# Optimization experiments

Hardware: AMD Instinct MI355X
Metric: run time of the kernel (lower is better)

Reference implementation:

```python
import jax, jax.numpy as jnp
import numpy as np

EMB = 300
NUM_LAYERS = 5
NUM_GRAPHS = 1024
NUM_JUNCTIONS = 8192
TEMP = 0.04
EPS = 1e-5
SELF_LOOP_BOND_TYPE = 4


def gcn_conv(x, edge_index, edge_attr, W, b, ee1, ee2):
    # pretrain-gnns GCNConv: add self-loops (bond type 4, direction 0),
    # degree-normalized add aggregation of (x_src + edge_emb).
    N = x.shape[0]
    loop = jnp.arange(N, dtype=edge_index.dtype)
    src = jnp.concatenate([edge_index[0], loop])
    dst = jnp.concatenate([edge_index[1], loop])
    bt = jnp.concatenate([edge_attr[:, 0], jnp.full((N,), SELF_LOOP_BOND_TYPE, edge_attr.dtype)])
    bd = jnp.concatenate([edge_attr[:, 1], jnp.zeros((N,), edge_attr.dtype)])
    eemb = ee1[bt] + ee2[bd]                                   # [E+N, D]
    deg = jax.ops.segment_sum(jnp.ones(src.shape, x.dtype), src, num_segments=N)
    dinv = jnp.where(deg > 0, 1.0 / jnp.sqrt(jnp.maximum(deg, 1e-12)), 0.0)
    norm = dinv[src] * dinv[dst]                               # [E+N]
    h = x @ W.T + b                                            # [N, D]
    msg = norm[:, None] * (h[src] + eemb)                      # gather + fuse
    return jax.ops.segment_sum(msg, dst, num_segments=N)      # scatter-add


def batchnorm(h, gamma, beta):
    mu = h.mean(0)
    var = h.var(0)
    return gamma * (h - mu) / jnp.sqrt(var + EPS) + beta


def gnn_encoder(x, edge_index, edge_attr, ae1, ae2, W, b, ee1, ee2, gamma, beta):
    h = ae1[x[:, 0]] + ae2[x[:, 1]]
    for l in range(NUM_LAYERS):
        h = gcn_conv(h, edge_index, edge_attr, W[l], b[l], ee1[l], ee2[l])
        h = batchnorm(h, gamma[l], beta[l])
        if l < NUM_LAYERS - 1:
            h = jax.nn.relu(h)
    return h


def junction_encoder(h, jW, jb, jee1, jee2):
    # SuperEncoder is called with empty edge_index -> only self-loops.
    empty_ei = jnp.zeros((2, 0), jnp.int32)
    empty_ea = jnp.zeros((0, 2), jnp.int32)
    h = jax.nn.relu(gcn_conv(h, empty_ei, empty_ea, jW[0], jb[0], jee1[0], jee2[0]))
    return gcn_conv(h, empty_ei, empty_ea, jW[1], jb[1], jee1[1], jee2[1])


def mean_pool(h, ids, num):
    s = jax.ops.segment_sum(h, ids, num_segments=num)
    c = jax.ops.segment_sum(jnp.ones((h.shape[0],), h.dtype), ids, num_segments=num)
    return s / jnp.maximum(c, 1.0)[:, None]


def l2norm(h):
    return h / jnp.maximum(jnp.linalg.norm(h, axis=1, keepdims=True), 1e-12)


def setup_inputs() -> dict:
    key = jax.random.key(0)
    ks = jax.random.split(key, 32)
    N, E = 200000, 400000
    inp = {
        'batch_x': jax.random.randint(ks[0], (N, 2), 0, 3, jnp.int32),
        'batch_edge_index': jax.random.randint(ks[1], (2, E), 0, N, jnp.int32),
        'batch_edge_attr': jax.random.randint(ks[2], (E, 2), 0, 3, jnp.int32),
        'batch_graph_ids': jax.random.randint(ks[3], (N,), 0, NUM_GRAPHS, jnp.int32),
        'frag_x': jax.random.randint(ks[4], (N, 2), 0, 3, jnp.int32),
        'frag_edge_index': jax.random.randint(ks[5], (2, E), 0, N, jnp.int32),
        'frag_edge_attr': jax.random.randint(ks[6], (E, 2), 0, 3, jnp.int32),
        'frag_junction_ids': jax.random.randint(ks[7], (N,), 0, NUM_JUNCTIONS, jnp.int32),
        'junction_graph_ids': jax.random.randint(ks[8], (NUM_JUNCTIONS,), 0, NUM_GRAPHS, jnp.int32),
        'junction_mask': jax.random.uniform(ks[9], (NUM_JUNCTIONS,), jnp.float32),
    }
    s = 0.05
    inp.update({
        'atom_emb1': jax.random.normal(ks[10], (120, EMB), jnp.float32) * s,
        'atom_emb2': jax.random.normal(ks[11], (3, EMB), jnp.float32) * s,
        'gnn_W': jax.random.normal(ks[12], (NUM_LAYERS, EMB, EMB), jnp.float32) * s,
        'gnn_b': jnp.zeros((NUM_LAYERS, EMB), jnp.float32),
        'gnn_ee1': jax.random.normal(ks[13], (NUM_LAYERS, 6, EMB), jnp.float32) * s,
        'gnn_ee2': jax.random.normal(ks[14], (NUM_LAYERS, 3, EMB), jnp.float32) * s,
        'bn_gamma': jnp.ones((NUM_LAYERS, EMB), jnp.float32),
        'bn_beta': jnp.zeros((NUM_LAYERS, EMB), jnp.float32),
        'jct_W': jax.random.normal(ks[15], (2, EMB, EMB), jnp.float32) * s,
        'jct_b': jnp.zeros((2, EMB), jnp.float32),
        'jct_ee1': jax.random.normal(ks[16], (2, 6, EMB), jnp.float32) * s,
        'jct_ee2': jax.random.normal(ks[17], (2, 3, EMB), jnp.float32) * s,
        'mask_embedding': jax.random.normal(ks[18], (EMB,), jnp.float32),
    })
    return inp


def reference(batch_x, batch_edge_index, batch_edge_attr, batch_graph_ids,
              frag_x, frag_edge_index, frag_edge_attr, frag_junction_ids,
              junction_graph_ids, junction_mask,
              atom_emb1, atom_emb2, gnn_W, gnn_b, gnn_ee1, gnn_ee2,
              bn_gamma, bn_beta, jct_W, jct_b, jct_ee1, jct_ee2, mask_embedding):
    # branch 0: whole molecules
    h = gnn_encoder(batch_x, batch_edge_index, batch_edge_attr,
                    atom_emb1, atom_emb2, gnn_W, gnn_b, gnn_ee1, gnn_ee2, bn_gamma, bn_beta)
    g = mean_pool(h, batch_graph_ids, NUM_GRAPHS)
    f0 = l2norm(junction_encoder(g, jct_W, jct_b, jct_ee1, jct_ee2))
    # branch 1: fragments -> junction nodes, masked overwrite, pooled per graph
    h = gnn_encoder(frag_x, frag_edge_index, frag_edge_attr,
                    atom_emb1, atom_emb2, gnn_W, gnn_b, gnn_ee1, gnn_ee2, bn_gamma, bn_beta)
    j = mean_pool(h, frag_junction_ids, NUM_JUNCTIONS)
    j = jnp.where(junction_mask[:, None] > 0.5, mask_embedding[None, :], j)
    j = junction_encoder(j, jct_W, jct_b, jct_ee1, jct_ee2)
    f1 = l2norm(mean_pool(j, junction_graph_ids, NUM_GRAPHS))
    logits = (f0 @ f1.T) / TEMP
    return logits
```

## Files before the change

kernel.cpp:

```cpp
#include <hip/hip_runtime.h>
#include <math.h>

#define EMBD 300
#define HROW 304
#define LDF  304
#define KEXT 320
#define BCH  80
#define BSTR 40
#define TS2  312
#define SPR  608
#define CE(a,b) (((a)+(b)-1)/(b))

typedef _Float16 h16;
typedef __attribute__((ext_vector_type(8))) _Float16 half8;
typedef __attribute__((ext_vector_type(4))) float f32x4;

__global__ void k_diag(float* out, int n, float v){
  int i = blockIdx.x*256 + threadIdx.x;
  if (i < n) out[i] = v;
}
__global__ void k_set_val(int* p, int n, int v){
  int i = blockIdx.x*256 + threadIdx.x;
  if (i < n) p[i] = v;
}
__global__ void k_count_src(const int* __restrict__ ei, int E, int* __restrict__ deg){
  int e = blockIdx.x*256 + threadIdx.x;
  if (e < E) atomicAdd(&deg[ei[e]], 1);
}
__global__ void k_dinv(const int* __restrict__ deg, float* __restrict__ dinv, int N){
  int i = blockIdx.x*256 + threadIdx.x;
  if (i < N) dinv[i] = 1.0f / sqrtf((float)(deg[i] + 1));
}
__global__ void k_count_dst(const int* __restrict__ ei, int E, int* __restrict__ counts){
  int e = blockIdx.x*256 + threadIdx.x;
  if (e < E) atomicAdd(&counts[ei[E + e]], 1);
}
__global__ void k_count_ids(const int* __restrict__ ids, int n, int* __restrict__ counts){
  int i = blockIdx.x*256 + threadIdx.x;
  if (i < n) atomicAdd(&counts[ids[i]], 1);
}
__global__ void k_scan_block(const int* __restrict__ in, int M, int* __restrict__ out, int* __restrict__ bsum){
  __shared__ int s[256];
  int t = threadIdx.x, i = blockIdx.x*256 + t;
  int v = (i < M) ? in[i] : 0;
  s[t] = v; __syncthreads();
  for (int off = 1; off < 256; off <<= 1){
    int x = (t >= off) ? s[t-off] : 0;
    __syncthreads();
    s[t] += x;
    __syncthreads();
  }
  if (i < M) out[i] = s[t] - v;
  if (t == 255) bsum[blockIdx.x] = s[255];
}
__global__ void k_scan_sums(int* __restrict__ bsum, int B){
  __shared__ int s[1024];
  int t = threadIdx.x;
  int v = (t < B) ? bsum[t] : 0;
  s[t] = v; __syncthreads();
  for (int off = 1; off < 1024; off <<= 1){
    int x = (t >= off) ? s[t-off] : 0;
    __syncthreads();
    s[t] += x;
    __syncthreads();
  }
  if (t < B) bsum[t] = s[t] - v;
}
__global__ void k_scan_add(int* __restrict__ out, const int* __restrict__ bsum, int M){
  int i = blockIdx.x*256 + threadIdx.x;
  if (i < M) out[i] += bsum[blockIdx.x];
}
__global__ void k_fill_edges(const int* __restrict__ ei, const int* __restrict__ ea, int E, int N,
                             const int* __restrict__ offs, int* __restrict__ cur, int* __restrict__ entries){
  int e = blockIdx.x*256 + threadIdx.x;
  if (e < E){
    int s  = ei[e];
    int d  = ei[E + e];
    int bt = ea[2*e], bd = ea[2*e + 1];
    int pos = offs[d] + atomicAdd(&cur[d], 1);
    entries[pos] = s | (bt << 20) | (bd << 23);
  } else if (e < E + N){
    int i = e - E;
    int pos = offs[i] + atomicAdd(&cur[i], 1);
    entries[pos] = i | (4 << 20);
  }
}
__global__ void k_fill_rows(const int* __restrict__ ids, int n, const int* __restrict__ offs,
                            int* __restrict__ cur, int* __restrict__ entries){
  int i = blockIdx.x*256 + threadIdx.x;
  if (i < n){
    int g = ids[i];
    int pos = offs[g] + atomicAdd(&cur[g], 1);
    entries[pos] = i;
  }
}

__global__ void k_init_h0(const int* __restrict__ x, const float* __restrict__ ae1,
                          const float* __restrict__ ae2, h16* __restrict__ h, int N){
  int i = blockIdx.x, t = threadIdx.x;
  int a = x[2*i], b = x[2*i + 1];
  const float* e1 = ae1 + (size_t)a*EMBD;
  const float* e2 = ae2 + (size_t)b*EMBD;
  h16* hr = h + (size_t)i*HROW;
  hr[t] = (h16)(e1[t] + e2[t]);
  int c = t + 256;
  if (c < HROW) hr[c] = (c < EMBD) ? (h16)(e1[c] + e2[c]) : (h16)0.f;
}

__global__ void k_wext(const float* __restrict__ W, const float* __restrict__ b,
                       const float* __restrict__ ee1, const float* __restrict__ ee2,
                       h16* __restrict__ out){
  int l = blockIdx.y, o = blockIdx.x, t = threadIdx.x;
  h16* d = out + ((size_t)l*KEXT + o)*KEXT;
  for (int k = t; k < KEXT; k += 256){
    float v = 0.f;
    if (o < EMBD){
      if      (k < EMBD)            v = W[(size_t)l*EMBD*EMBD + (size_t)o*EMBD + k];
      else if (k == 304)            v = b[l*EMBD + o];
      else if (k >= 305 && k < 311) v = ee1[((size_t)l*6 + (k-305))*EMBD + o];
      else if (k >= 311 && k < 314) v = ee2[((size_t)l*3 + (k-311))*EMBD + o];
    }
    d[k] = (h16)v;
  }
}

__global__ void k_id_coef(float* coef, h16* coefh){
  int c = blockIdx.x*256 + threadIdx.x;
  if (c < HROW){
    coef[c] = (c < EMBD) ? 1.f : 0.f;
    coef[HROW + c] = 0.f;
  }
  if (c < KEXT){
    coefh[c] = (c < EMBD) ? (h16)1.f : (h16)0.f;
    coefh[KEXT + c] = (h16)0.f;
  }
}
__global__ void k_bn_coef(const float* __restrict__ stats, const float* __restrict__ gamma,
                          const float* __restrict__ beta, float* __restrict__ coef,
                          h16* __restrict__ coefh, float invN){
  int c = blockIdx.x*256 + threadIdx.x;
  if (c >= KEXT) return;
  float sc = 0.f, sh = 0.f;
  if (c < EMBD){
    float mu  = stats[c]*invN;
    float var = stats[EMBD + c]*invN - mu*mu;
    sc = gamma[c]*rsqrtf(var + 1e-5f);
    sh = beta[c] - mu*sc;
  }
  if (c < HROW){ coef[c] = sc; coef[HROW + c] = sh; }
  coefh[c] = (h16)sc; coefh[KEXT + c] = (h16)sh;
}

__global__ void k_red_stats(const h16* __restrict__ spart, int nb, float* __restrict__ stats){
  int t = threadIdx.x;
  int c1 = t + 256;
  float a0 = 0.f, q0 = 0.f, a1 = 0.f, q1 = 0.f;
  for (int b = blockIdx.x; b < nb; b += gridDim.x){
    const h16* sp = spart + (size_t)b*SPR;
    a0 += (float)sp[t];
    q0 += (float)sp[304 + t];
    if (c1 < EMBD){ a1 += (float)sp[c1]; q1 += (float)sp[304 + c1]; }
  }
  if (t < EMBD){ atomicAdd(&stats[t], a0); atomicAdd(&stats[EMBD + t], q0); }
  if (c1 < EMBD){ atomicAdd(&stats[c1], a1); atomicAdd(&stats[EMBD + c1], q1); }
}

template<int RELU>
__global__ void __launch_bounds__(256)
k_layer(const h16* __restrict__ hRaw, const h16* __restrict__ coefh,
        const float* __restrict__ dinv,
        const int* __restrict__ offs, const int* __restrict__ counts,
        const int* __restrict__ entries, const h16* __restrict__ Wx,
        h16* __restrict__ hOut, int N, h16* __restrict__ spart)
{
  __shared__ h16  tile[64][TS2];
  __shared__ h16  Bs[BCH][BSTR];
  __shared__ float sred[2*HROW];
  __shared__ int   rstart[64];
  __shared__ int   rcnt[64];
  __shared__ float dvv[64];

  int tid = threadIdx.x;
  int wid = tid >> 6, lane = tid & 63;
  int m16 = lane & 15, ko = lane >> 4;
  long row0 = (long)blockIdx.x * 64;

  if (tid < 64){
    long g = row0 + tid;
    int o = 0, c = 0; float d = 0.f;
    if (g < N){ o = offs[g]; c = counts[g]; d = dinv[g]; }
    rstart[tid] = o; rcnt[tid] = c; dvv[tid] = d;
  }
  for (int i = tid; i < 2*HROW; i += 256) sred[i] = 0.f;
  __syncthreads();

  int lr = wid*16 + m16;
  int myStart = rstart[lr], myCnt = rcnt[lr];
  float di = dvv[lr];

  int srcA[8]; float wvA[8]; int eA[8];
  #pragma unroll
  for (int j = 0; j < 8; j++){
    int e = entries[myStart + j];
    bool act = j < myCnt;
    int s = act ? (e & 0xFFFFF) : N;
    float wv = dinv[act ? s : 0];
    wvA[j] = act ? wv : 0.f;
    srcA[j] = s; eA[j] = e;
  }
  float ext[8] = {0,0,0,0,0,0,0,0};
  if (ko >= 2){
    int extbase = (ko - 2)*8;
    #pragma unroll
    for (int j = 0; j < 8; j++){
      unsigned msk = 1u | (1u << (1 + ((eA[j] >> 20) & 7))) | (1u << (7 + ((eA[j] >> 23) & 3)));
      #pragma unroll
      for (int c = 0; c < 8; c++)
        ext[c] += ((msk >> (extbase + c)) & 1u) ? wvA[j] : 0.f;
    }
  }
  half8 wvh[8];
  #pragma unroll
  for (int j = 0; j < 8; j++){
    _Float16 w = (_Float16)wvA[j];
    #pragma unroll
    for (int c = 0; c < 8; c++) wvh[j][c] = w;
  }

  half8 acc[10];
  #pragma unroll
  for (int k = 0; k < 10; k++) acc[k] = (half8)(_Float16)0;

  if (__any(myCnt > 8)){
    for (int j = 8; j < myCnt; j++){
      int e = entries[myStart + j];
      int s = e & 0xFFFFF;
      float wv = dinv[s];
      if (ko >= 2){
        int extbase = (ko - 2)*8;
        unsigned msk = 1u | (1u << (1 + ((e >> 20) & 7))) | (1u << (7 + ((e >> 23) & 3)));
        #pragma unroll
        for (int c = 0; c < 8; c++)
          ext[c] += ((msk >> (extbase + c)) & 1u) ? wv : 0.f;
      }
      _Float16 wh = (_Float16)wv;
      half8 w8;
      #pragma unroll
      for (int c = 0; c < 8; c++) w8[c] = wh;
      #pragma unroll
      for (int k = 0; k < 10; k++){
        if (k == 9 && ko >= 2) break;
        half8 sck = *(const half8*)&coefh[k*32 + ko*8];
        half8 shk = *(const half8*)&coefh[KEXT + k*32 + ko*8];
        half8 x = *(const half8*)(hRaw + (size_t)s*HROW + k*32 + ko*8);
        half8 y = sck*x + shk;
        if (RELU){
          #pragma unroll
          for (int c = 0; c < 8; c++) y[c] = y[c] > (_Float16)0 ? y[c] : (_Float16)0;
        }
        acc[k] += w8*y;
      }
    }
  }

  #pragma unroll
  for (int k = 0; k < 9; k++){
    half8 sck = *(const half8*)&coefh[k*32 + ko*8];
    half8 shk = *(const half8*)&coefh[KEXT + k*32 + ko*8];
    half8 a = acc[k];
    #pragma unroll
    for (int j = 0; j < 8; j++){
      half8 x = *(const half8*)(hRaw + (size_t)srcA[j]*HROW + k*32 + ko*8);
      half8 y = sck*x + shk;
      if (RELU){
        #pragma unroll
        for (int c = 0; c < 8; c++) y[c] = y[c] > (_Float16)0 ? y[c] : (_Float16)0;
      }
      a += wvh[j]*y;
    }
    acc[k] = a;
  }
  {
    half8 a = acc[9];
    if (ko < 2){
      half8 sck = *(const half8*)&coefh[288 + ko*8];
      half8 shk = *(const half8*)&coefh[KEXT + 288 + ko*8];
      #pragma unroll
      for (int j = 0; j < 8; j++){
        half8 x = *(const half8*)(hRaw + (size_t)srcA[j]*HROW + 288 + ko*8);
        half8 y = sck*x + shk;
        if (RELU){
          #pragma unroll
          for (int c = 0; c < 8; c++) y[c] = y[c] > (_Float16)0 ? y[c] : (_Float16)0;
        }
        a += wvh[j]*y;
      }
    } else {
      #pragma unroll
      for (int c = 0; c < 8; c++) a[c] += (_Float16)ext[c];
    }
    acc[9] = a;
  }

  half8 afr[10];
  {
    _Float16 dh = (_Float16)di;
    half8 d8;
    #pragma unroll
    for (int c = 0; c < 8; c++) d8[c] = dh;
    #pragma unroll
    for (int k = 0; k < 10; k++) afr[k] = acc[k] * d8;
  }

  int cr = ko * 4;
  #pragma unroll
  for (int jt = 0; jt < 4; jt++){
    f32x4 a2[5];
    #pragma unroll
    for (int j = 0; j < 5; j++) a2[j] = (f32x4){0.f,0.f,0.f,0.f};
    for (int k0 = 0; k0 < 10; k0++){
      __syncthreads();
      for (int idx = tid; idx < 320; idx += 256){
        int o = idx >> 2, qd = (idx & 3) * 8;
        *(half8*)&Bs[o][qd] = *(const half8*)(Wx + (size_t)(jt*BCH + o)*KEXT + k0*32 + qd);
      }
      __syncthreads();
      #pragma unroll
      for (int j = 0; j < 5; j++){
        half8 bfr = *(const half8*)&Bs[j*16 + m16][ko*8];
        a2[j] = __builtin_amdgcn_mfma_f32_16x16x32_f16(afr[k0], bfr, a2[j], 0, 0, 0);
      }
    }
    #pragma unroll
    for (int j = 0; j < 5; j++){
      int col = jt*BCH + j*16 + m16;
      float s = 0.f, q = 0.f;
      #pragma unroll
      for (int r = 0; r < 4; r++){
        float v = a2[j][r];
        s += v; q += v*v;
      }
      s += __shfl_xor(s, 16, 64); s += __shfl_xor(s, 32, 64);
      q += __shfl_xor(q, 16, 64); q += __shfl_xor(q, 32, 64);
      if (ko == 0 && col < EMBD){
        atomicAdd(&sred[col], s);
        atomicAdd(&sred[HROW + col], q);
      }
    }
    #pragma unroll
    for (int j = 0; j < 5; j++){
      int col = jt*BCH + j*16 + m16;
      if (col < HROW){
        #pragma unroll
        for (int r = 0; r < 4; r++)
          tile[wid*16 + cr + r][col] = (h16)a2[j][r];
      }
    }
  }
  __syncthreads();
  for (int idx = tid; idx < 64*38; idx += 256){
    int row = idx / 38, c = idx - row*38;
    long grow = row0 + row;
    if (grow < N)
      *(uint4*)(hOut + grow*HROW + c*8) = *(const uint4*)&tile[row][c*8];
  }
  h16* sp = spart + (size_t)blockIdx.x*SPR;
  for (int c = tid; c < EMBD; c += 256){
    sp[c]       = (h16)sred[c];
    sp[304 + c] = (h16)sred[HROW + c];
  }
}

__global__ void k_pool_h(const h16* __restrict__ h, const int* __restrict__ offs,
                         const int* __restrict__ counts, const int* __restrict__ entries,
                         float* __restrict__ out, int M){
  int g = blockIdx.x, t = threadIdx.x, c1 = t + 256;
  int off = offs[g], cnt = counts[g];
  float a0 = 0.f, a1 = 0.f;
  for (int j = 0; j < cnt; j++){
    int r = entries[off + j];
    const h16* hr = h + (size_t)r*HROW;
    a0 += (float)hr[t];
    if (c1 < EMBD) a1 += (float)hr[c1];
  }
  float inv = 1.0f / fmaxf((float)cnt, 1.0f);
  float* o = out + (size_t)g*LDF;
  o[t] = a0*inv;
  if (c1 < EMBD) o[c1] = a1*inv;
}
__global__ void k_pool_f32(const float* __restrict__ h, const int* __restrict__ offs,
                           const int* __restrict__ counts, const int* __restrict__ entries,
                           float* __restrict__ out, int M){
  int g = blockIdx.x, t = threadIdx.x, c1 = t + 256;
  int off = offs[g], cnt = counts[g];
  float a0 = 0.f, a1 = 0.f;
  for (int j = 0; j < cnt; j++){
    int r = entries[off + j];
    const float* hr = h + (size_t)r*LDF;
    a0 += hr[t];
    if (c1 < EMBD) a1 += hr[c1];
  }
  float inv = 1.0f / fmaxf((float)cnt, 1.0f);
  float* o = out + (size_t)g*LDF;
  o[t] = a0*inv;
  if (c1 < EMBD) o[c1] = a1*inv;
}

__global__ void k_affine_rows(float* __restrict__ rows, const float* __restrict__ coef, int M){
  int g = blockIdx.x, t = threadIdx.x, c1 = t + 256;
  float* r = rows + (size_t)g*LDF;
  r[t] = coef[t]*r[t] + coef[HROW + t];
  if (c1 < EMBD) r[c1] = coef[c1]*r[c1] + coef[HROW + c1];
}

__global__ void k_mask(float* __restrict__ j, const float* __restrict__ mask,
                       const float* __restrict__ memb, int M){
  int i = blockIdx.x;
  if (mask[i] <= 0.5f) return;
  int t = threadIdx.x, c1 = t + 256;
  float* jr = j + (size_t)i*LDF;
  jr[t] = memb[t];
  if (c1 < EMBD) jr[c1] = memb[c1];
}

__global__ void k_l2norm(float* __restrict__ f, int M){
  int g = blockIdx.x, t = threadIdx.x, c1 = t + 256;
  float* fr = f + (size_t)g*LDF;
  float v0 = fr[t];
  float v1 = (c1 < EMBD) ? fr[c1] : 0.f;
  float ss = v0*v0 + v1*v1;
  #pragma unroll
  for (int o = 32; o > 0; o >>= 1) ss += __shfl_down(ss, o, 64);
  __shared__ float red[4];
  int wid = t >> 6, lane = t & 63;
  if (lane == 0) red[wid] = ss;
  __syncthreads();
  if (t == 0) red[0] = 1.0f / fmaxf(sqrtf(red[0]+red[1]+red[2]+red[3]), 1e-12f);
  __syncthreads();
  float inv = red[0];
  fr[t] = v0*inv;
  if (c1 < EMBD) fr[c1] = v1*inv;
}

__global__ void __launch_bounds__(256)
k_gemm(const float* __restrict__ A, int lda, const float* __restrict__ W, int ldw,
       const float* __restrict__ bias, const float* __restrict__ e1, const float* __restrict__ e2,
       float* __restrict__ C, int ldc, int M, int Ncols, int K, int relu, float scale){
  __shared__ float As[16][68];
  __shared__ float Ws[16][68];
  int row0 = blockIdx.y * 64, col0 = blockIdx.x * 64;
  int tid = threadIdx.x;
  int tx = tid & 15, ty = tid >> 4;
  float acc[4][4] = {};
  for (int k0 = 0; k0 < K; k0 += 16){
    int r  = tid >> 2;
    int kk = (tid & 3) * 4;
    int gk = k0 + kk;
    float v[4] = {0.f,0.f,0.f,0.f};
    int gr = row0 + r;
    if (gr < M){
      if (gk + 3 < K){ float4 f = *(const float4*)(A + (size_t)gr*lda + gk); v[0]=f.x;v[1]=f.y;v[2]=f.z;v[3]=f.w; }
      else for (int j = 0; j < 4; j++) if (gk + j < K) v[j] = A[(size_t)gr*lda + gk + j];
    }
    As[kk+0][r]=v[0]; As[kk+1][r]=v[1]; As[kk+2][r]=v[2]; As[kk+3][r]=v[3];
    float w[4] = {0.f,0.f,0.f,0.f};
    int o = col0 + r;
    if (o < Ncols){
      if (gk + 3 < K){ float4 f = *(const float4*)(W + (size_t)o*ldw + gk); w[0]=f.x;w[1]=f.y;w[2]=f.z;w[3]=f.w; }
      else for (int j = 0; j < 4; j++) if (gk + j < K) w[j] = W[(size_t)o*ldw + gk + j];
    }
    Ws[kk+0][r]=w[0]; Ws[kk+1][r]=w[1]; Ws[kk+2][r]=w[2]; Ws[kk+3][r]=w[3];
    __syncthreads();
    #pragma unroll
    for (int k = 0; k < 16; k++){
      float4 a4 = *(const float4*)&As[k][ty*4];
      float4 b4 = *(const float4*)&Ws[k][tx*4];
      float a[4] = {a4.x,a4.y,a4.z,a4.w};
      float b[4] = {b4.x,b4.y,b4.z,b4.w};
      #pragma unroll
      for (int i = 0; i < 4; i++)
        #pragma unroll
        for (int j = 0; j < 4; j++) acc[i][j] += a[i]*b[j];
    }
    __syncthreads();
  }
  #pragma unroll
  for (int i = 0; i < 4; i++){
    int rr = row0 + ty*4 + i;
    if (rr >= M) continue;
    #pragma unroll
    for (int j = 0; j < 4; j++){
      int cc = col0 + tx*4 + j;
      if (cc >= Ncols) continue;
      float v = acc[i][j];
      if (bias) v += bias[cc];
      if (e1)   v += e1[cc];
      if (e2)   v += e2[cc];
      v *= scale;
      if (relu) v = fmaxf(v, 0.f);
      C[(size_t)rr*ldc + cc] = v;
    }
  }
}

static inline void scan_excl(const int* counts, int M, int* offs, int* bsum, hipStream_t s){
  int B = CE(M, 256);
  k_scan_block<<<B,256,0,s>>>(counts, M, offs, bsum);
  k_scan_sums<<<1,1024,0,s>>>(bsum, B);
  k_scan_add<<<B,256,0,s>>>(offs, bsum, M);
}
static inline void gemm_f32(const float* A,int lda,const float* W,int ldw,
                            const float* bias,const float* e1,const float* e2,
                            float* C,int ldc,int M,int Ncols,int K,
                            int relu,float scale,hipStream_t s){
  dim3 grid(CE(Ncols,64), CE(M,64));
  k_gemm<<<grid,256,0,s>>>(A,lda,W,ldw,bias,e1,e2,C,ldc,M,Ncols,K,relu,scale);
}

extern "C" void kernel_launch(void* const* d_in, const int* in_sizes, int n_in,
                              void* d_out, int out_size, void* d_ws, size_t ws_size,
                              hipStream_t stream) {
  const int*   batch_x   = (const int*)d_in[0];
  const int*   batch_ei  = (const int*)d_in[1];
  const int*   batch_ea  = (const int*)d_in[2];
  const int*   batch_gid = (const int*)d_in[3];
  const int*   frag_x    = (const int*)d_in[4];
  const int*   frag_ei   = (const int*)d_in[5];
  const int*   frag_ea   = (const int*)d_in[6];
  const int*   frag_jid  = (const int*)d_in[7];
  const int*   jct_gid   = (const int*)d_in[8];
  const float* jct_mask  = (const float*)d_in[9];
  const float* ae1       = (const float*)d_in[10];
  const float* ae2       = (const float*)d_in[11];
  const float* gnn_W     = (const float*)d_in[12];
  const float* gnn_b     = (const float*)d_in[13];
  const float* gnn_ee1   = (const float*)d_in[14];
  const float* gnn_ee2   = (const float*)d_in[15];
  const float* bn_gamma  = (const float*)d_in[16];
  const float* bn_beta   = (const float*)d_in[17];
  const float* jct_W     = (const float*)d_in[18];
  const float* jct_b     = (const float*)d_in[19];
  const float* jct_ee1   = (const float*)d_in[20];
  const float* jct_ee2   = (const float*)d_in[21];
  const float* mask_emb  = (const float*)d_in[22];

  const int N = in_sizes[0] / 2;
  const int E = in_sizes[1] / 2;
  const int NG = 1024, NJ = 8192;
  const int LBLK = CE(N, 64);

  size_t off = 0;
  char* base = (char*)d_ws;
  auto carve = [&](size_t bytes) -> void* {
    void* p = base + off;
    off += (bytes + 255) & ~(size_t)255;
    return p;
  };
  h16*  hA      = (h16*) carve((size_t)(N+1) * HROW * 2);
  h16*  hB      = (h16*) carve((size_t)(N+1) * HROW * 2);
  float* dinv    = (float*)carve((size_t)N * 4);
  int*   degcnt  = (int*)  carve((size_t)N * 4);
  int*   cursor  = degcnt;
  int*   counts  = (int*)  carve((size_t)N * 4);
  int*   offs    = (int*)  carve((size_t)(N + 1) * 4);
  int*   entries = (int*)  carve((size_t)(E + N) * 4);
  int*   bsum    = (int*)  carve(1024 * 4);
  float* stats   = (float*)carve(2 * EMBD * 4);
  float* coef    = (float*)carve(2 * HROW * 4);
  float* idcoef  = (float*)carve(2 * HROW * 4);
  h16*  coefh   = (h16*) carve(2 * KEXT * 2);
  h16*  idcoefh = (h16*) carve(2 * KEXT * 2);
  h16*  wext    = (h16*) carve((size_t)5 * KEXT * KEXT * 2);
  float* f0      = (float*)carve((size_t)NG * LDF * 4);
  float* f1      = (float*)carve((size_t)NG * LDF * 4);
  h16*  spart   = (h16*) carve((size_t)LBLK * SPR * 2);
  size_t required = off;
  float* g0      = (float*)hA;
  float* t1      = (float*)((char*)hA + ((size_t)16 << 20));
  float* t2      = (float*)((char*)hA + ((size_t)32 << 20));
  (void)n_in;

  if (ws_size < required || d_ws == nullptr){
    float v = 1.0e6f + (float)(ws_size >> 20) * 1000.0f;
    k_diag<<<CE(out_size,256),256,0,stream>>>((float*)d_out, out_size, v);
    return;
  }

  { dim3 g(KEXT, 5); k_wext<<<g,256,0,stream>>>(gnn_W, gnn_b, gnn_ee1, gnn_ee2, wext); }
  k_id_coef<<<CE(KEXT,256),256,0,stream>>>(idcoef, idcoefh);
  hipMemsetAsync(hA + (size_t)N*HROW, 0, HROW*2, stream);
  hipMemsetAsync(hB + (size_t)N*HROW, 0, HROW*2, stream);

  for (int br = 0; br < 2; br++){
    const int* x  = br ? frag_x  : batch_x;
    const int* ei = br ? frag_ei : batch_ei;
    const int* ea = br ? frag_ea : batch_ea;

    hipMemsetAsync(degcnt, 0, (size_t)N*4, stream);
    k_count_src<<<CE(E,256),256,0,stream>>>(ei, E, degcnt);
    k_dinv<<<CE(N,256),256,0,stream>>>(degcnt, dinv, N);

    k_set_val<<<CE(N,256),256,0,stream>>>(counts, N, 1);
    k_count_dst<<<CE(E,256),256,0,stream>>>(ei, E, counts);
    scan_excl(counts, N, offs, bsum, stream);
    hipMemsetAsync(cursor, 0, (size_t)N*4, stream);
    k_fill_edges<<<CE(E+N,256),256,0,stream>>>(ei, ea, E, N, offs, cursor, entries);

    k_init_h0<<<N,256,0,stream>>>(x, ae1, ae2, hA, N);

    for (int l = 0; l < 5; l++){
      const h16* src = (l & 1) ? hB : hA;
      h16*       dst = (l & 1) ? hA : hB;
      const h16* ch  = (l == 0) ? idcoefh : coefh;
      hipMemsetAsync(stats, 0, 2*EMBD*4, stream);
      if (l == 0)
        k_layer<0><<<LBLK,256,0,stream>>>(src, ch, dinv, offs, counts, entries,
                                          wext + (size_t)l*KEXT*KEXT, dst, N, spart);
      else
        k_layer<1><<<LBLK,256,0,stream>>>(src, ch, dinv, offs, counts, entries,
                                          wext + (size_t)l*KEXT*KEXT, dst, N, spart);
      k_red_stats<<<64,256,0,stream>>>(spart, LBLK, stats);
      k_bn_coef<<<CE(KEXT,256),256,0,stream>>>(stats, bn_gamma + l*EMBD, bn_beta + l*EMBD,
                                               coef, coefh, 1.0f/(float)N);
    }

    if (br == 0){
      hipMemsetAsync(counts, 0, (size_t)NG*4, stream);
      k_count_ids<<<CE(N,256),256,0,stream>>>(batch_gid, N, counts);
      scan_excl(counts, NG, offs, bsum, stream);
      hipMemsetAsync(cursor, 0, (size_t)NG*4, stream);
      k_fill_rows<<<CE(N,256),256,0,stream>>>(batch_gid, N, offs, cursor, entries);
      k_pool_h<<<NG,256,0,stream>>>(hB, offs, counts, entries, g0, NG);
      k_affine_rows<<<NG,256,0,stream>>>(g0, coef, NG);
      gemm_f32(g0, LDF, jct_W, EMBD, jct_b,
               jct_ee1 + 4*EMBD, jct_ee2,
               t1, LDF, NG, EMBD, EMBD, 1, 1.0f, stream);
      gemm_f32(t1, LDF, jct_W + EMBD*EMBD, EMBD, jct_b + EMBD,
               jct_ee1 + 6*EMBD + 4*EMBD, jct_ee2 + 3*EMBD,
               f0, LDF, NG, EMBD, EMBD, 0, 1.0f, stream);
      k_l2norm<<<NG,256,0,stream>>>(f0, NG);
    } else {
      hipMemsetAsync(counts, 0, (size_t)NJ*4, stream);
      k_count_ids<<<CE(N,256),256,0,stream>>>(frag_jid, N, counts);
      scan_excl(counts, NJ, offs, bsum, stream);
      hipMemsetAsync(cursor, 0, (size_t)NJ*4, stream);
      k_fill_rows<<<CE(N,256),256,0,stream>>>(frag_jid, N, offs, cursor, entries);
      k_pool_h<<<NJ,256,0,stream>>>(hB, offs, counts, entries, t1, NJ);
      k_affine_rows<<<NJ,256,0,stream>>>(t1, coef, NJ);
      k_mask<<<NJ,256,0,stream>>>(t1, jct_mask, mask_emb, NJ);
      gemm_f32(t1, LDF, jct_W, EMBD, jct_b,
               jct_ee1 + 4*EMBD, jct_ee2,
               t2, LDF, NJ, EMBD, EMBD, 1, 1.0f, stream);
      gemm_f32(t2, LDF, jct_W + EMBD*EMBD, EMBD, jct_b + EMBD,
               jct_ee1 + 6*EMBD + 4*EMBD, jct_ee2 + 3*EMBD,
               t1, LDF, NJ, EMBD, EMBD, 0, 1.0f, stream);
      hipMemsetAsync(counts, 0, (size_t)NG*4, stream);
      k_count_ids<<<CE(NJ,256),256,0,stream>>>(jct_gid, NJ, counts);
      scan_excl(counts, NG, offs, bsum, stream);
      hipMemsetAsync(cursor, 0, (size_t)NG*4, stream);
      k_fill_rows<<<CE(NJ,256),256,0,stream>>>(jct_gid, NJ, offs, cursor, entries);
      k_pool_f32<<<NG,256,0,stream>>>(t1, offs, counts, entries, f1, NG);
      k_l2norm<<<NG,256,0,stream>>>(f1, NG);
    }
  }

  gemm_f32(f0, LDF, f1, LDF, nullptr, nullptr, nullptr,
           (float*)d_out, 1024, NG, NG, EMBD, 0, 25.0f, stream);
}
```

Baseline: 4.033 ms.

## Use MFMA fp16 GEMM for junction layers and fuse pool/affine/mask kernels

Replaces the fp32 scalar GEMMs in the junction encoder with an MFMA f16 kernel that keeps A fragments in registers and uses padded fp16 copies of the junction weights. It also fuses the BN affine transform and the mask overwrite into the pooling kernel, unrolls the pooling gather by four, and merges the source- and destination-degree counting into one kernel. This cuts launch count and the extra memory passes over the pooled rows, at the cost of fp16 rounding on the junction GEMM inputs.

```diff
diff --git a/kernel.cpp b/kernel.cpp
--- a/kernel.cpp
+++ b/kernel.cpp
@@ -23,17 +23,17 @@
   int i = blockIdx.x*256 + threadIdx.x;
   if (i < n) p[i] = v;
 }
-__global__ void k_count_src(const int* __restrict__ ei, int E, int* __restrict__ deg){
+__global__ void k_count_both(const int* __restrict__ ei, int E,
+                             int* __restrict__ deg, int* __restrict__ cnts){
   int e = blockIdx.x*256 + threadIdx.x;
-  if (e < E) atomicAdd(&deg[ei[e]], 1);
+  if (e < E){
+    atomicAdd(&deg[ei[e]], 1);
+    atomicAdd(&cnts[ei[E + e]], 1);
+  }
 }
 __global__ void k_dinv(const int* __restrict__ deg, float* __restrict__ dinv, int N){
   int i = blockIdx.x*256 + threadIdx.x;
   if (i < N) dinv[i] = 1.0f / sqrtf((float)(deg[i] + 1));
-}
-__global__ void k_count_dst(const int* __restrict__ ei, int E, int* __restrict__ counts){
-  int e = blockIdx.x*256 + threadIdx.x;
-  if (e < E) atomicAdd(&counts[ei[E + e]], 1);
 }
 __global__ void k_count_ids(const int* __restrict__ ids, int n, int* __restrict__ counts){
   int i = blockIdx.x*256 + threadIdx.x;
@@ -122,6 +122,12 @@
     }
     d[k] = (h16)v;
   }
+}
+__global__ void k_wpad(const float* __restrict__ W, h16* __restrict__ out){
+  int l = blockIdx.y, o = blockIdx.x, t = threadIdx.x;
+  h16* d = out + ((size_t)l*KEXT + o)*KEXT;
+  for (int k = t; k < KEXT; k += 256)
+    d[k] = (h16)((o < EMBD && k < EMBD) ? W[(size_t)l*EMBD*EMBD + (size_t)o*EMBD + k] : 0.f);
 }
 
 __global__ void k_id_coef(float* coef, h16* coefh){
@@ -373,20 +379,44 @@
 
 __global__ void k_pool_h(const h16* __restrict__ h, const int* __restrict__ offs,
                          const int* __restrict__ counts, const int* __restrict__ entries,
-                         float* __restrict__ out, int M){
+                         float* __restrict__ out, const float* __restrict__ coef,
+                         const float* __restrict__ mask, const float* __restrict__ memb){
   int g = blockIdx.x, t = threadIdx.x, c1 = t + 256;
   int off = offs[g], cnt = counts[g];
   float a0 = 0.f, a1 = 0.f;
-  for (int j = 0; j < cnt; j++){
+  int j = 0;
+  for (; j + 4 <= cnt; j += 4){
+    int r0 = entries[off+j],   r1 = entries[off+j+1];
+    int r2 = entries[off+j+2], r3 = entries[off+j+3];
+    const h16* p0 = h + (size_t)r0*HROW;
+    const h16* p1 = h + (size_t)r1*HROW;
+    const h16* p2 = h + (size_t)r2*HROW;
+    const h16* p3 = h + (size_t)r3*HROW;
+    float x0 = (float)p0[t], x1 = (float)p1[t];
+    float x2 = (float)p2[t], x3 = (float)p3[t];
+    a0 += (x0 + x1) + (x2 + x3);
+    if (c1 < EMBD){
+      float y0 = (float)p0[c1], y1 = (float)p1[c1];
+      float y2 = (float)p2[c1], y3 = (float)p3[c1];
+      a1 += (y0 + y1) + (y2 + y3);
+    }
+  }
+  for (; j < cnt; j++){
     int r = entries[off + j];
     const h16* hr = h + (size_t)r*HROW;
     a0 += (float)hr[t];
     if (c1 < EMBD) a1 += (float)hr[c1];
   }
   float inv = 1.0f / fmaxf((float)cnt, 1.0f);
+  float v0 = coef[t]*(a0*inv) + coef[HROW + t];
+  float v1 = (c1 < EMBD) ? coef[c1]*(a1*inv) + coef[HROW + c1] : 0.f;
+  if (mask && mask[g] > 0.5f){
+    v0 = memb[t];
+    if (c1 < EMBD) v1 = memb[c1];
+  }
   float* o = out + (size_t)g*LDF;
-  o[t] = a0*inv;
-  if (c1 < EMBD) o[c1] = a1*inv;
+  o[t] = v0;
+  if (c1 < EMBD) o[c1] = v1;
 }
 __global__ void k_pool_f32(const float* __restrict__ h, const int* __restrict__ offs,
                            const int* __restrict__ counts, const int* __restrict__ entries,
@@ -406,23 +436,6 @@
   if (c1 < EMBD) o[c1] = a1*inv;
 }
 
-__global__ void k_affine_rows(float* __restrict__ rows, const float* __restrict__ coef, int M){
-  int g = blockIdx.x, t = threadIdx.x, c1 = t + 256;
-  float* r = rows + (size_t)g*LDF;
-  r[t] = coef[t]*r[t] + coef[HROW + t];
-  if (c1 < EMBD) r[c1] = coef[c1]*r[c1] + coef[HROW + c1];
-}
-
-__global__ void k_mask(float* __restrict__ j, const float* __restrict__ mask,
-                       const float* __restrict__ memb, int M){
-  int i = blockIdx.x;
-  if (mask[i] <= 0.5f) return;
-  int t = threadIdx.x, c1 = t + 256;
-  float* jr = j + (size_t)i*LDF;
-  jr[t] = memb[t];
-  if (c1 < EMBD) jr[c1] = memb[c1];
-}
-
 __global__ void k_l2norm(float* __restrict__ f, int M){
   int g = blockIdx.x, t = threadIdx.x, c1 = t + 256;
   float* fr = f + (size_t)g*LDF;
@@ -440,6 +453,74 @@
   float inv = red[0];
   fr[t] = v0*inv;
   if (c1 < EMBD) fr[c1] = v1*inv;
+}
+
+__global__ void __launch_bounds__(256)
+k_gemm16(const float* __restrict__ A, int lda, const h16* __restrict__ Wp,
+         const float* __restrict__ bias, const float* __restrict__ e1, const float* __restrict__ e2,
+         float* __restrict__ C, int ldc, int M, int Ncols, int relu)
+{
+  __shared__ h16 Bs[BCH][BSTR];
+  int tid = threadIdx.x;
+  int wid = tid >> 6, lane = tid & 63;
+  int m16 = lane & 15, ko = lane >> 4;
+  int row0 = blockIdx.y * 64;
+  int col0 = blockIdx.x * BCH;
+  int arow = row0 + wid*16 + m16;
+  bool rok = arow < M;
+  const float* Ar = A + (size_t)(rok ? arow : 0) * lda;
+
+  half8 afr[10];
+  #pragma unroll
+  for (int k0 = 0; k0 < 9; k0++){
+    const float* p = Ar + k0*32 + ko*8;
+    float4 fa = rok ? *(const float4*)p       : (float4){0.f,0.f,0.f,0.f};
+    float4 fb = rok ? *(const float4*)(p + 4) : (float4){0.f,0.f,0.f,0.f};
+    half8 v;
+    v[0]=(h16)fa.x; v[1]=(h16)fa.y; v[2]=(h16)fa.z; v[3]=(h16)fa.w;
+    v[4]=(h16)fb.x; v[5]=(h16)fb.y; v[6]=(h16)fb.z; v[7]=(h16)fb.w;
+    afr[k0] = v;
+  }
+  {
+    half8 v;
+    #pragma unroll
+    for (int c = 0; c < 8; c++){
+      int ch = 288 + ko*8 + c;
+      v[c] = (h16)((rok && ch < EMBD) ? Ar[ch] : 0.f);
+    }
+    afr[9] = v;
+  }
+
+  f32x4 a2[5];
+  #pragma unroll
+  for (int j = 0; j < 5; j++) a2[j] = (f32x4){0.f,0.f,0.f,0.f};
+  for (int k0 = 0; k0 < 10; k0++){
+    __syncthreads();
+    for (int idx = tid; idx < 320; idx += 256){
+      int o = idx >> 2, qd = (idx & 3) * 8;
+      *(half8*)&Bs[o][qd] = *(const half8*)(Wp + (size_t)(col0 + o)*KEXT + k0*32 + qd);
+    }
+    __syncthreads();
+    #pragma unroll
+    for (int j = 0; j < 5; j++){
+      half8 bfr = *(const half8*)&Bs[j*16 + m16][ko*8];
+      a2[j] = __builtin_amdgcn_mfma_f32_16x16x32_f16(afr[k0], bfr, a2[j], 0, 0, 0);
+    }
+  }
+  #pragma unroll
+  for (int j = 0; j < 5; j++){
+    int cc = col0 + j*16 + m16;
+    if (cc >= Ncols) continue;
+    float add = bias[cc] + e1[cc] + e2[cc];
+    #pragma unroll
+    for (int r = 0; r < 4; r++){
+      int rr = row0 + wid*16 + ko*4 + r;
+      if (rr >= M) continue;
+      float v = a2[j][r] + add;
+      if (relu) v = fmaxf(v, 0.f);
+      C[(size_t)rr*ldc + cc] = v;
+    }
+  }
 }
 
 __global__ void __launch_bounds__(256)
@@ -509,12 +590,11 @@
   k_scan_sums<<<1,1024,0,s>>>(bsum, B);
   k_scan_add<<<B,256,0,s>>>(offs, bsum, M);
 }
-static inline void gemm_f32(const float* A,int lda,const float* W,int ldw,
-                            const float* bias,const float* e1,const float* e2,
-                            float* C,int ldc,int M,int Ncols,int K,
-                            int relu,float scale,hipStream_t s){
-  dim3 grid(CE(Ncols,64), CE(M,64));
-  k_gemm<<<grid,256,0,s>>>(A,lda,W,ldw,bias,e1,e2,C,ldc,M,Ncols,K,relu,scale);
+static inline void gemm16(const float* A, const h16* Wp,
+                          const float* bias, const float* e1, const float* e2,
+                          float* C, int M, int relu, hipStream_t s){
+  dim3 grid(CE(EMBD, BCH), CE(M, 64));
+  k_gemm16<<<grid,256,0,s>>>(A, LDF, Wp, bias, e1, e2, C, LDF, M, EMBD, relu);
 }
 
 extern "C" void kernel_launch(void* const* d_in, const int* in_sizes, int n_in,
@@ -571,6 +651,7 @@
   h16*  coefh   = (h16*) carve(2 * KEXT * 2);
   h16*  idcoefh = (h16*) carve(2 * KEXT * 2);
   h16*  wext    = (h16*) carve((size_t)5 * KEXT * KEXT * 2);
+  h16*  wjx     = (h16*) carve((size_t)2 * KEXT * KEXT * 2);
   float* f0      = (float*)carve((size_t)NG * LDF * 4);
   float* f1      = (float*)carve((size_t)NG * LDF * 4);
   h16*  spart   = (h16*) carve((size_t)LBLK * SPR * 2);
@@ -587,6 +668,7 @@
   }
 
   { dim3 g(KEXT, 5); k_wext<<<g,256,0,stream>>>(gnn_W, gnn_b, gnn_ee1, gnn_ee2, wext); }
+  { dim3 g(KEXT, 2); k_wpad<<<g,256,0,stream>>>(jct_W, wjx); }
   k_id_coef<<<CE(KEXT,256),256,0,stream>>>(idcoef, idcoefh);
   hipMemsetAsync(hA + (size_t)N*HROW, 0, HROW*2, stream);
   hipMemsetAsync(hB + (size_t)N*HROW, 0, HROW*2, stream);
@@ -597,11 +679,9 @@
     const int* ea = br ? frag_ea : batch_ea;
 
     hipMemsetAsync(degcnt, 0, (size_t)N*4, stream);
-    k_count_src<<<CE(E,256),256,0,stream>>>(ei, E, degcnt);
+    k_set_val<<<CE(N,256),256,0,stream>>>(counts, N, 1);
+    k_count_both<<<CE(E,256),256,0,stream>>>(ei, E, degcnt, counts);
     k_dinv<<<CE(N,256),256,0,stream>>>(degcnt, dinv, N);
-
-    k_set_val<<<CE(N,256),256,0,stream>>>(counts, N, 1);
-    k_count_dst<<<CE(E,256),256,0,stream>>>(ei, E, counts);
     scan_excl(counts, N, offs, bsum, stream);
     hipMemsetAsync(cursor, 0, (size_t)N*4, stream);
     k_fill_edges<<<CE(E+N,256),256,0,stream>>>(ei, ea, E, N, offs, cursor, entries);
@@ -630,14 +710,11 @@
       scan_excl(counts, NG, offs, bsum, stream);
       hipMemsetAsync(cursor, 0, (size_t)NG*4, stream);
       k_fill_rows<<<CE(N,256),256,0,stream>>>(batch_gid, N, offs, cursor, entries);
-      k_pool_h<<<NG,256,0,stream>>>(hB, offs, counts, entries, g0, NG);
-      k_affine_rows<<<NG,256,0,stream>>>(g0, coef, NG);
-      gemm_f32(g0, LDF, jct_W, EMBD, jct_b,
-               jct_ee1 + 4*EMBD, jct_ee2,
-               t1, LDF, NG, EMBD, EMBD, 1, 1.0f, stream);
-      gemm_f32(t1, LDF, jct_W + EMBD*EMBD, EMBD, jct_b + EMBD,
-               jct_ee1 + 6*EMBD + 4*EMBD, jct_ee2 + 3*EMBD,
-               f0, LDF, NG, EMBD, EMBD, 0, 1.0f, stream);
+      k_pool_h<<<NG,256,0,stream>>>(hB, offs, counts, entries, g0, coef, nullptr, nullptr);
+      gemm16(g0, wjx,
+             jct_b, jct_ee1 + 4*EMBD, jct_ee2, t1, NG, 1, stream);
+      gemm16(t1, wjx + (size_t)KEXT*KEXT,
+             jct_b + EMBD, jct_ee1 + 6*EMBD + 4*EMBD, jct_ee2 + 3*EMBD, f0, NG, 0, stream);
       k_l2norm<<<NG,256,0,stream>>>(f0, NG);
     } else {
       hipMemsetAsync(counts, 0, (size_t)NJ*4, stream);
@@ -645,15 +722,11 @@
       scan_excl(counts, NJ, offs, bsum, stream);
       hipMemsetAsync(cursor, 0, (size_t)NJ*4, stream);
       k_fill_rows<<<CE(N,256),256,0,stream>>>(frag_jid, N, offs, cursor, entries);
-      k_pool_h<<<NJ,256,0,stream>>>(hB, offs, counts, entries, t1, NJ);
-      k_affine_rows<<<NJ,256,0,stream>>>(t1, coef, NJ);
-      k_mask<<<NJ,256,0,stream>>>(t1, jct_mask, mask_emb, NJ);
-      gemm_f32(t1, LDF, jct_W, EMBD, jct_b,
-               jct_ee1 + 4*EMBD, jct_ee2,
-               t2, LDF, NJ, EMBD, EMBD, 1, 1.0f, stream);
-      gemm_f32(t2, LDF, jct_W + EMBD*EMBD, EMBD, jct_b + EMBD,
-               jct_ee1 + 6*EMBD + 4*EMBD, jct_ee2 + 3*EMBD,
-               t1, LDF, NJ, EMBD, EMBD, 0, 1.0f, stream);
+      k_pool_h<<<NJ,256,0,stream>>>(hB, offs, counts, entries, t1, coef, jct_mask, mask_emb);
+      gemm16(t1, wjx,
+             jct_b, jct_ee1 + 4*EMBD, jct_ee2, t2, NJ, 1, stream);
+      gemm16(t2, wjx + (size_t)KEXT*KEXT,
+             jct_b + EMBD, jct_ee1 + 6*EMBD + 4*EMBD, jct_ee2 + 3*EMBD, t1, NJ, 0, stream);
       hipMemsetAsync(counts, 0, (size_t)NG*4, stream);
       k_count_ids<<<CE(NJ,256),256,0,stream>>>(jct_gid, NJ, counts);
       scan_excl(counts, NG, offs, bsum, stream);
@@ -664,6 +737,9 @@
     }
   }
 
-  gemm_f32(f0, LDF, f1, LDF, nullptr, nullptr, nullptr,
-           (float*)d_out, 1024, NG, NG, EMBD, 0, 25.0f, stream);
-}
+  {
+    dim3 grid(CE(NG,64), CE(NG,64));
+    k_gemm<<<grid,256,0,stream>>>(f0, LDF, f1, LDF, nullptr, nullptr, nullptr,
+                                  (float*)d_out, 1024, NG, NG, EMBD, 0, 25.0f);
+  }
+}
```

Measured after the change: 3.893 ms. -3.5%, faster.
